# Kernel tuning notes

Hardware: AMD Instinct MI355X
Metric: run time of the kernel (lower is better)

## Reference

```python
import jax, jax.numpy as jnp
import numpy as np

B, N, E, F, H = 4, 10000, 320000, 128, 128


def setup_inputs() -> dict:
    key = jax.random.key(0)
    ks = jax.random.split(key, 12)
    s = 1.0 / np.sqrt(F)
    sh = 1.0 / np.sqrt(H)
    return {
        "batch_feat": jax.random.normal(ks[0], (B, N, F), dtype=jnp.float32),
        "batch_edges": jax.random.randint(ks[1], (B, 2, E), 0, N, dtype=jnp.int32),
        "batch_attr": jax.random.uniform(ks[2], (B, E), dtype=jnp.float32),
        "W1": jax.random.uniform(ks[3], (F, H), jnp.float32, -s, s),
        "b1": jnp.zeros((H,), jnp.float32),
        "W2": jax.random.uniform(ks[4], (H, H), jnp.float32, -sh, sh),
        "b2": jnp.zeros((H,), jnp.float32),
        "W3": jax.random.uniform(ks[5], (H, H), jnp.float32, -sh, sh),
        "b3": jnp.zeros((H,), jnp.float32),
        "Wl": jax.random.uniform(ks[6], (H, 1), jnp.float32, -sh, sh),
        "bl": jnp.zeros((1,), jnp.float32),
    }


def reference(batch_feat, batch_edges, batch_attr, W1, b1, W2, b2, W3, b3, Wl, bl):
    n_nodes = batch_feat.shape[1]

    def gcn_conv(x, row, col, w, W, b):
        # PyG gcn_norm with add_self_loops=False: deg = scatter_add(w, col)
        deg = jax.ops.segment_sum(w, col, num_segments=n_nodes)  # [N]
        dinv = jnp.where(deg > 0, jax.lax.rsqrt(deg), 0.0)
        norm = dinv[row] * w * dinv[col]                         # [E]
        xw = x @ W                                               # [N,H]
        msg = norm[:, None] * xw[row]                            # gather [E,H]
        return jax.ops.segment_sum(msg, col, num_segments=n_nodes) + b

    def per_graph(x, ei, w):
        row, col = ei[0], ei[1]
        h = jax.nn.relu(gcn_conv(x, row, col, w, W1, b1))
        h = jax.nn.relu(gcn_conv(h, row, col, w, W2, b2))
        h = jax.nn.relu(gcn_conv(h, row, col, w, W3, b3))
        return h.mean(axis=0) @ Wl + bl                          # [1]

    return jax.vmap(per_graph)(batch_feat, batch_edges, batch_attr)  # [B,1]
```

## Files before the change

### kernel.cpp

```cpp
#include <hip/hip_runtime.h>

#define BB 4
#define NN 10000
#define EE 320000
#define HH 128
#define HALFN 5000
#define NK2 (2 * NN)
#define RS (2 * NN + 1)
#define NHB 64
#define EPB (EE / NHB)

__global__ __launch_bounds__(256) void hist_kernel(
    const int* __restrict__ edges, unsigned short* __restrict__ hb,
    unsigned short* __restrict__ lrank) {
  __shared__ int lh[NN];
  int b = blockIdx.y;
  int blk = blockIdx.x;
  int t = threadIdx.x;
  const int* rows = edges + (size_t)b * 2 * EE;
  const int* cols = rows + EE;
#pragma unroll
  for (int half = 0; half < 2; ++half) {
    for (int i = t; i < NN; i += 256) lh[i] = 0;
    __syncthreads();
    for (int i = t; i < EPB; i += 256) {
      int e = blk * EPB + i;
      int row = rows[e];
      int col = cols[e];
      if ((row >= HALFN) == (half != 0)) {
        int lr = atomicAdd(&lh[col], 1);
        lrank[(size_t)b * EE + e] = (unsigned short)lr;
      }
    }
    __syncthreads();
    unsigned short* hbrow = hb + ((size_t)(b * NHB + blk)) * NK2 + half * NN;
    for (int i = t; i < NN; i += 256) hbrow[i] = (unsigned short)lh[i];
    __syncthreads();
  }
}

__global__ __launch_bounds__(256) void colscan_kernel(
    unsigned short* __restrict__ hb, int* __restrict__ cnt) {
  int b = blockIdx.y;
  int k = blockIdx.x * 256 + threadIdx.x;
  if (k >= NK2) return;
  int acc = 0;
  for (int j = 0; j < NHB; ++j) {
    size_t idx = ((size_t)(b * NHB + j)) * NK2 + k;
    int v = hb[idx];
    hb[idx] = (unsigned short)acc;
    acc += v;
  }
  cnt[b * NK2 + k] = acc;
}

__global__ __launch_bounds__(256) void scan_kernel(
    const int* __restrict__ cnt, int* __restrict__ rowstart) {
  int b = blockIdx.x, t = threadIdx.x;
  __shared__ int s[256];
  int running = 0;
  for (int base = 0; base < NK2; base += 2048) {
    int v[8];
    int i0 = base + t * 8;
    int tsum = 0;
#pragma unroll
    for (int j = 0; j < 8; ++j) {
      v[j] = (i0 + j < NK2) ? cnt[b * NK2 + i0 + j] : 0;
      tsum += v[j];
    }
    s[t] = tsum;
    __syncthreads();
    for (int o = 1; o < 256; o <<= 1) {
      int add = (t >= o) ? s[t - o] : 0;
      __syncthreads();
      s[t] += add;
      __syncthreads();
    }
    int ex = running + s[t] - tsum;
#pragma unroll
    for (int j = 0; j < 8; ++j) {
      if (i0 + j < NK2) rowstart[b * RS + i0 + j] = ex;
      ex += v[j];
    }
    int tot = s[255];
    __syncthreads();
    running += tot;
  }
  if (t == 0) rowstart[b * RS + NK2] = running;
}

__global__ __launch_bounds__(256) void fill_kernel(
    const int* __restrict__ edges, const float* __restrict__ attr,
    const unsigned short* __restrict__ lrank, const unsigned short* __restrict__ hb,
    const int* __restrict__ rowstart, int2* __restrict__ csr) {
  int b = blockIdx.y;
  int e0 = (blockIdx.x * 256 + threadIdx.x) * 2;
  int blk = e0 / EPB;
  int2 rr = *(const int2*)(edges + (size_t)b * 2 * EE + e0);
  int2 cc = *(const int2*)(edges + (size_t)b * 2 * EE + EE + e0);
  float2 ww = *(const float2*)(attr + (size_t)b * EE + e0);
  unsigned int lr2 = *(const unsigned int*)(lrank + (size_t)b * EE + e0);
  int k0 = ((rr.x >= HALFN) ? NN : 0) + cc.x;
  int k1 = ((rr.y >= HALFN) ? NN : 0) + cc.y;
  const unsigned short* hbrow = hb + ((size_t)(b * NHB + blk)) * NK2;
  int p0 = rowstart[b * RS + k0] + (int)hbrow[k0] + (int)(lr2 & 0xffffu);
  int p1 = rowstart[b * RS + k1] + (int)hbrow[k1] + (int)(lr2 >> 16);
  csr[(size_t)b * EE + p0] = make_int2(rr.x, __float_as_int(ww.x));
  csr[(size_t)b * EE + p1] = make_int2(rr.y, __float_as_int(ww.y));
}

__global__ __launch_bounds__(256) void deg_kernel(
    const int2* __restrict__ csr, const int* __restrict__ rowstart,
    float* __restrict__ dinv) {
  int b = blockIdx.y;
  int n = blockIdx.x * 256 + threadIdx.x;
  if (n >= NN) return;
  const int2* c = csr + (size_t)b * EE;
  float sum = 0.f;
#pragma unroll
  for (int q = 0; q < 2; ++q) {
    int key = q * NN + n;
    int s0 = rowstart[b * RS + key], s1 = rowstart[b * RS + key + 1];
    for (int i = s0; i < s1; ++i) sum += __int_as_float(c[i].y);
  }
  dinv[b * NN + n] = sum > 0.f ? rsqrtf(sum) : 0.f;
}

__global__ __launch_bounds__(256) void gemm_kernel(
    const float* __restrict__ xsrc, const float* __restrict__ p0,
    const float* __restrict__ p1, const float* __restrict__ dinv,
    const float* __restrict__ xbias, const float* __restrict__ W,
    float* __restrict__ out, int fused) {
  __shared__ float xs[32 * 68];
  __shared__ float ws[32 * 144];
  int b = blockIdx.y;
  int row0 = blockIdx.x * 64;
  int t = threadIdx.x;
  int rg = t >> 4, cg = t & 15;
  int fc = cg * 8 + ((cg >> 2) << 2);
  float acc[4][8];
#pragma unroll
  for (int r = 0; r < 4; ++r)
#pragma unroll
    for (int j = 0; j < 8; ++j) acc[r][j] = 0.f;
  size_t gbase = (size_t)b * NN * HH;

  for (int k0 = 0; k0 < HH; k0 += 32) {
#pragma unroll
    for (int i = 0; i < 2; ++i) {
      int idx = t + i * 256;
      int rl = idx >> 3, kq = idx & 7;
      int row = row0 + rl;
      float4 v = make_float4(0.f, 0.f, 0.f, 0.f);
      if (row < NN) {
        size_t o = gbase + (size_t)row * HH + k0 + kq * 4;
        if (fused) {
          float4 u0 = *(const float4*)(p0 + o);
          float4 u1 = *(const float4*)(p1 + o);
          float dn = dinv[b * NN + row];
          float4 bb = *(const float4*)(xbias + k0 + kq * 4);
          v.x = fmaxf((u0.x + u1.x) * dn + bb.x, 0.f);
          v.y = fmaxf((u0.y + u1.y) * dn + bb.y, 0.f);
          v.z = fmaxf((u0.z + u1.z) * dn + bb.z, 0.f);
          v.w = fmaxf((u0.w + u1.w) * dn + bb.w, 0.f);
        } else {
          v = *(const float4*)(xsrc + o);
        }
      }
      xs[(kq * 4 + 0) * 68 + rl] = v.x;
      xs[(kq * 4 + 1) * 68 + rl] = v.y;
      xs[(kq * 4 + 2) * 68 + rl] = v.z;
      xs[(kq * 4 + 3) * 68 + rl] = v.w;
    }
#pragma unroll
    for (int i = 0; i < 4; ++i) {
      int idx = t + i * 256;
      int kk = idx >> 5, c = (idx & 31) * 4;
      float4 v = *(const float4*)(W + (size_t)(k0 + kk) * HH + c);
      int f = c + ((c >> 5) << 2);
      *(float4*)&ws[kk * 144 + f] = v;
    }
    __syncthreads();
#pragma unroll 4
    for (int k = 0; k < 32; ++k) {
      float4 xv = *(const float4*)&xs[k * 68 + rg * 4];
      float4 w0 = *(const float4*)&ws[k * 144 + fc];
      float4 w1 = *(const float4*)&ws[k * 144 + fc + 4];
      const float* xp = (const float*)&xv;
#pragma unroll
      for (int r = 0; r < 4; ++r) {
        acc[r][0] += xp[r] * w0.x; acc[r][1] += xp[r] * w0.y;
        acc[r][2] += xp[r] * w0.z; acc[r][3] += xp[r] * w0.w;
        acc[r][4] += xp[r] * w1.x; acc[r][5] += xp[r] * w1.y;
        acc[r][6] += xp[r] * w1.z; acc[r][7] += xp[r] * w1.w;
      }
    }
    __syncthreads();
  }
#pragma unroll
  for (int r = 0; r < 4; ++r) {
    int row = row0 + rg * 4 + r;
    if (row < NN) {
      float* og = out + gbase + (size_t)row * HH + cg * 8;
      *(float4*)og = make_float4(acc[r][0], acc[r][1], acc[r][2], acc[r][3]);
      *(float4*)(og + 4) = make_float4(acc[r][4], acc[r][5], acc[r][6], acc[r][7]);
    }
  }
}

__global__ __launch_bounds__(256) void agg_kernel(
    const float* __restrict__ xw, const int2* __restrict__ csr,
    const int* __restrict__ rowstart, const float* __restrict__ dinv,
    float* __restrict__ p0g, float* __restrict__ p1g) {
  int g = blockIdx.x & 7;
  int b = g >> 1;
  int q = g & 1;
  int chunk = blockIdx.x >> 3;
  int half = (threadIdx.x >> 5) & 1;
  int n = chunk * 8 + (threadIdx.x >> 6) * 2 + half;
  int sl = threadIdx.x & 31;
  int key = q * NN + n;
  int s0 = rowstart[b * RS + key], s1 = rowstart[b * RS + key + 1];
  const float* xwg = xw + (size_t)b * NN * HH;
  const float* dv = dinv + b * NN;
  const int2* c = csr + (size_t)b * EE;
  float4 a0 = make_float4(0.f, 0.f, 0.f, 0.f);
  float4 a1 = make_float4(0.f, 0.f, 0.f, 0.f);
  float4 a2 = make_float4(0.f, 0.f, 0.f, 0.f);
  float4 a3 = make_float4(0.f, 0.f, 0.f, 0.f);
  int i = s0;
  for (; i + 4 <= s1; i += 4) {
    int2 e0 = c[i];
    int2 e1 = c[i + 1];
    int2 e2 = c[i + 2];
    int2 e3 = c[i + 3];
    float w0 = __int_as_float(e0.y) * dv[e0.x];
    float w1 = __int_as_float(e1.y) * dv[e1.x];
    float w2 = __int_as_float(e2.y) * dv[e2.x];
    float w3 = __int_as_float(e3.y) * dv[e3.x];
    float4 v0 = *(const float4*)(xwg + (size_t)e0.x * HH + sl * 4);
    float4 v1 = *(const float4*)(xwg + (size_t)e1.x * HH + sl * 4);
    float4 v2 = *(const float4*)(xwg + (size_t)e2.x * HH + sl * 4);
    float4 v3 = *(const float4*)(xwg + (size_t)e3.x * HH + sl * 4);
    a0.x += w0 * v0.x; a0.y += w0 * v0.y; a0.z += w0 * v0.z; a0.w += w0 * v0.w;
    a1.x += w1 * v1.x; a1.y += w1 * v1.y; a1.z += w1 * v1.z; a1.w += w1 * v1.w;
    a2.x += w2 * v2.x; a2.y += w2 * v2.y; a2.z += w2 * v2.z; a2.w += w2 * v2.w;
    a3.x += w3 * v3.x; a3.y += w3 * v3.y; a3.z += w3 * v3.z; a3.w += w3 * v3.w;
  }
  for (; i < s1; ++i) {
    int2 e0 = c[i];
    float w0 = __int_as_float(e0.y) * dv[e0.x];
    float4 v0 = *(const float4*)(xwg + (size_t)e0.x * HH + sl * 4);
    a0.x += w0 * v0.x; a0.y += w0 * v0.y; a0.z += w0 * v0.z; a0.w += w0 * v0.w;
  }
  a0.x += a1.x + a2.x + a3.x;
  a0.y += a1.y + a2.y + a3.y;
  a0.z += a1.z + a2.z + a3.z;
  a0.w += a1.w + a2.w + a3.w;
  float* pq = (q == 0) ? p0g : p1g;
  *(float4*)(pq + ((size_t)b * NN + n) * HH + sl * 4) = a0;
}

__global__ __launch_bounds__(64) void init_out_kernel(float* out, const float* __restrict__ bl) {
  if (threadIdx.x < BB) out[threadIdx.x] = bl[0];
}

__global__ __launch_bounds__(256) void final_kernel(
    const float* __restrict__ p0g, const float* __restrict__ p1g,
    const float* __restrict__ dinv, const float* __restrict__ b3,
    const float* __restrict__ Wl, float* __restrict__ out) {
  int b = blockIdx.y;
  int t = threadIdx.x;
  int f = t & 127;
  int rr = t >> 7;
  float bf = b3[f];
  const float* dv = dinv + b * NN;
  float p = 0.f;
  for (int n = blockIdx.x * 2 + rr; n < NN; n += gridDim.x * 2) {
    size_t o = ((size_t)b * NN + n) * HH + f;
    p += fmaxf((p0g[o] + p1g[o]) * dv[n] + bf, 0.f);
  }
  __shared__ float s[256];
  s[t] = p;
  __syncthreads();
  float v = 0.f;
  if (t < 128) v = (s[t] + s[t + 128]) * Wl[f];
  __syncthreads();
  s[t] = v;
  __syncthreads();
  for (int o = 64; o > 0; o >>= 1) {
    if (t < o) s[t] += s[t + o];
    __syncthreads();
  }
  if (t == 0) atomicAdd(&out[b], s[0] * (1.0f / NN));
}

extern "C" void kernel_launch(void* const* d_in, const int* in_sizes, int n_in,
                              void* d_out, int out_size, void* d_ws, size_t ws_size,
                              hipStream_t stream) {
  const float* feat = (const float*)d_in[0];
  const int* edges = (const int*)d_in[1];
  const float* attr = (const float*)d_in[2];
  const float* W1 = (const float*)d_in[3];
  const float* b1 = (const float*)d_in[4];
  const float* W2 = (const float*)d_in[5];
  const float* b2 = (const float*)d_in[6];
  const float* W3 = (const float*)d_in[7];
  const float* b3 = (const float*)d_in[8];
  const float* Wl = (const float*)d_in[9];
  const float* bl = (const float*)d_in[10];
  float* out = (float*)d_out;

  char* ws = (char*)d_ws;
  size_t off = 0;
  auto alloc = [&](size_t bytes) {
    size_t o = off;
    off = (off + bytes + 255) & ~(size_t)255;
    return o;
  };
  int*   cnt      = (int*)  (ws + alloc((size_t)BB * NK2 * 4));
  int*   rowstart = (int*)  (ws + alloc((size_t)BB * RS * 4));
  int2*  csr      = (int2*) (ws + alloc((size_t)BB * EE * 8));
  float* xw       = (float*)(ws + alloc((size_t)BB * NN * HH * 4));
  float* p0       = (float*)(ws + alloc((size_t)BB * NN * HH * 4));
  float* p1       = (float*)(ws + alloc((size_t)BB * NN * HH * 4));
  unsigned short* lrank = (unsigned short*)xw;
  unsigned short* hb    = (unsigned short*)p0;
  float* dinv = (float*)cnt;

  dim3 hgrid(NHB, BB);
  hist_kernel<<<hgrid, 256, 0, stream>>>(edges, hb, lrank);
  colscan_kernel<<<dim3((NK2 + 255) / 256, BB), 256, 0, stream>>>(hb, cnt);
  scan_kernel<<<BB, 256, 0, stream>>>(cnt, rowstart);
  dim3 egrid2(EE / 512, BB);
  fill_kernel<<<egrid2, 256, 0, stream>>>(edges, attr, lrank, hb, rowstart, csr);
  deg_kernel<<<dim3((NN + 255) / 256, BB), 256, 0, stream>>>(csr, rowstart, dinv);

  dim3 ggrid((NN + 63) / 64, BB);
  int agrid = 8 * (NN / 8);

  gemm_kernel<<<ggrid, 256, 0, stream>>>(feat, nullptr, nullptr, nullptr, nullptr, W1, xw, 0);
  agg_kernel<<<agrid, 256, 0, stream>>>(xw, csr, rowstart, dinv, p0, p1);
  gemm_kernel<<<ggrid, 256, 0, stream>>>(nullptr, p0, p1, dinv, b1, W2, xw, 1);
  agg_kernel<<<agrid, 256, 0, stream>>>(xw, csr, rowstart, dinv, p0, p1);
  gemm_kernel<<<ggrid, 256, 0, stream>>>(nullptr, p0, p1, dinv, b2, W3, xw, 1);
  agg_kernel<<<agrid, 256, 0, stream>>>(xw, csr, rowstart, dinv, p0, p1);

  init_out_kernel<<<1, 64, 0, stream>>>(out, bl);
  final_kernel<<<dim3(64, BB), 256, 0, stream>>>(p0, p1, dinv, b3, Wl, out);
}
```

Before: 347.0 us.

## Compute degree during histogram, prefold dinv into CSR weights, use nontemporal access

```diff
diff --git a/kernel.cpp b/kernel.cpp
--- a/kernel.cpp
+++ b/kernel.cpp
@@ -10,52 +10,66 @@
 #define NHB 64
 #define EPB (EE / NHB)
 
+typedef int i32x2 __attribute__((ext_vector_type(2)));
+typedef float f32x4 __attribute__((ext_vector_type(4)));
+
 __global__ __launch_bounds__(256) void hist_kernel(
-    const int* __restrict__ edges, unsigned short* __restrict__ hb,
+    const int* __restrict__ edges, const float* __restrict__ attr,
+    unsigned short* __restrict__ hb, float* __restrict__ wsp,
     unsigned short* __restrict__ lrank) {
   __shared__ int lh[NN];
-  int b = blockIdx.y;
-  int blk = blockIdx.x;
-  int t = threadIdx.x;
+  __shared__ float lw[NN];
+  int b = blockIdx.y, blk = blockIdx.x, t = threadIdx.x;
   const int* rows = edges + (size_t)b * 2 * EE;
   const int* cols = rows + EE;
+  const float* wa = attr + (size_t)b * EE;
 #pragma unroll
   for (int half = 0; half < 2; ++half) {
-    for (int i = t; i < NN; i += 256) lh[i] = 0;
+    for (int i = t; i < NN; i += 256) { lh[i] = 0; lw[i] = 0.f; }
     __syncthreads();
     for (int i = t; i < EPB; i += 256) {
       int e = blk * EPB + i;
       int row = rows[e];
-      int col = cols[e];
       if ((row >= HALFN) == (half != 0)) {
+        int col = cols[e];
         int lr = atomicAdd(&lh[col], 1);
+        atomicAdd(&lw[col], wa[e]);
         lrank[(size_t)b * EE + e] = (unsigned short)lr;
       }
     }
     __syncthreads();
     unsigned short* hbrow = hb + ((size_t)(b * NHB + blk)) * NK2 + half * NN;
-    for (int i = t; i < NN; i += 256) hbrow[i] = (unsigned short)lh[i];
+    float* wsrow = wsp + ((size_t)(b * NHB + blk)) * NK2 + half * NN;
+    for (int i = t; i < NN; i += 256) {
+      hbrow[i] = (unsigned short)lh[i];
+      wsrow[i] = lw[i];
+    }
     __syncthreads();
   }
 }
 
 __global__ __launch_bounds__(256) void colscan_kernel(
-    unsigned short* __restrict__ hb, int* __restrict__ cnt) {
+    unsigned short* __restrict__ hb, const float* __restrict__ wsp,
+    int* __restrict__ cnt, float* __restrict__ wtot) {
   int b = blockIdx.y;
   int k = blockIdx.x * 256 + threadIdx.x;
   if (k >= NK2) return;
   int acc = 0;
+  float f = 0.f;
   for (int j = 0; j < NHB; ++j) {
     size_t idx = ((size_t)(b * NHB + j)) * NK2 + k;
     int v = hb[idx];
     hb[idx] = (unsigned short)acc;
     acc += v;
+    f += wsp[idx];
   }
   cnt[b * NK2 + k] = acc;
+  wtot[b * NK2 + k] = f;
 }
 
 __global__ __launch_bounds__(256) void scan_kernel(
-    const int* __restrict__ cnt, int* __restrict__ rowstart) {
+    const int* __restrict__ cnt, const float* __restrict__ wtot,
+    int* __restrict__ rowstart, float* __restrict__ dinv) {
   int b = blockIdx.x, t = threadIdx.x;
   __shared__ int s[256];
   int running = 0;
@@ -87,12 +101,17 @@
     running += tot;
   }
   if (t == 0) rowstart[b * RS + NK2] = running;
+  for (int i = t; i < NN; i += 256) {
+    float sm = wtot[b * NK2 + i] + wtot[b * NK2 + NN + i];
+    dinv[b * NN + i] = sm > 0.f ? rsqrtf(sm) : 0.f;
+  }
 }
 
 __global__ __launch_bounds__(256) void fill_kernel(
     const int* __restrict__ edges, const float* __restrict__ attr,
     const unsigned short* __restrict__ lrank, const unsigned short* __restrict__ hb,
-    const int* __restrict__ rowstart, int2* __restrict__ csr) {
+    const int* __restrict__ rowstart, const float* __restrict__ dinv,
+    int2* __restrict__ csr) {
   int b = blockIdx.y;
   int e0 = (blockIdx.x * 256 + threadIdx.x) * 2;
   int blk = e0 / EPB;
@@ -105,25 +124,12 @@
   const unsigned short* hbrow = hb + ((size_t)(b * NHB + blk)) * NK2;
   int p0 = rowstart[b * RS + k0] + (int)hbrow[k0] + (int)(lr2 & 0xffffu);
   int p1 = rowstart[b * RS + k1] + (int)hbrow[k1] + (int)(lr2 >> 16);
-  csr[(size_t)b * EE + p0] = make_int2(rr.x, __float_as_int(ww.x));
-  csr[(size_t)b * EE + p1] = make_int2(rr.y, __float_as_int(ww.y));
-}
-
-__global__ __launch_bounds__(256) void deg_kernel(
-    const int2* __restrict__ csr, const int* __restrict__ rowstart,
-    float* __restrict__ dinv) {
-  int b = blockIdx.y;
-  int n = blockIdx.x * 256 + threadIdx.x;
-  if (n >= NN) return;
-  const int2* c = csr + (size_t)b * EE;
-  float sum = 0.f;
-#pragma unroll
-  for (int q = 0; q < 2; ++q) {
-    int key = q * NN + n;
-    int s0 = rowstart[b * RS + key], s1 = rowstart[b * RS + key + 1];
-    for (int i = s0; i < s1; ++i) sum += __int_as_float(c[i].y);
-  }
-  dinv[b * NN + n] = sum > 0.f ? rsqrtf(sum) : 0.f;
+  float w0 = ww.x * dinv[b * NN + rr.x];
+  float w1 = ww.y * dinv[b * NN + rr.y];
+  i32x2 v0; v0.x = rr.x; v0.y = __float_as_int(w0);
+  i32x2 v1; v1.x = rr.y; v1.y = __float_as_int(w1);
+  __builtin_nontemporal_store(v0, (i32x2*)(csr + (size_t)b * EE + p0));
+  __builtin_nontemporal_store(v1, (i32x2*)(csr + (size_t)b * EE + p1));
 }
 
 __global__ __launch_bounds__(256) void gemm_kernel(
@@ -210,7 +216,7 @@
 
 __global__ __launch_bounds__(256) void agg_kernel(
     const float* __restrict__ xw, const int2* __restrict__ csr,
-    const int* __restrict__ rowstart, const float* __restrict__ dinv,
+    const int* __restrict__ rowstart,
     float* __restrict__ p0g, float* __restrict__ p1g) {
   int g = blockIdx.x & 7;
   int b = g >> 1;
@@ -222,7 +228,6 @@
   int key = q * NN + n;
   int s0 = rowstart[b * RS + key], s1 = rowstart[b * RS + key + 1];
   const float* xwg = xw + (size_t)b * NN * HH;
-  const float* dv = dinv + b * NN;
   const int2* c = csr + (size_t)b * EE;
   float4 a0 = make_float4(0.f, 0.f, 0.f, 0.f);
   float4 a1 = make_float4(0.f, 0.f, 0.f, 0.f);
@@ -230,14 +235,14 @@
   float4 a3 = make_float4(0.f, 0.f, 0.f, 0.f);
   int i = s0;
   for (; i + 4 <= s1; i += 4) {
-    int2 e0 = c[i];
-    int2 e1 = c[i + 1];
-    int2 e2 = c[i + 2];
-    int2 e3 = c[i + 3];
-    float w0 = __int_as_float(e0.y) * dv[e0.x];
-    float w1 = __int_as_float(e1.y) * dv[e1.x];
-    float w2 = __int_as_float(e2.y) * dv[e2.x];
-    float w3 = __int_as_float(e3.y) * dv[e3.x];
+    i32x2 e0 = __builtin_nontemporal_load((const i32x2*)(c + i));
+    i32x2 e1 = __builtin_nontemporal_load((const i32x2*)(c + i + 1));
+    i32x2 e2 = __builtin_nontemporal_load((const i32x2*)(c + i + 2));
+    i32x2 e3 = __builtin_nontemporal_load((const i32x2*)(c + i + 3));
+    float w0 = __int_as_float(e0.y);
+    float w1 = __int_as_float(e1.y);
+    float w2 = __int_as_float(e2.y);
+    float w3 = __int_as_float(e3.y);
     float4 v0 = *(const float4*)(xwg + (size_t)e0.x * HH + sl * 4);
     float4 v1 = *(const float4*)(xwg + (size_t)e1.x * HH + sl * 4);
     float4 v2 = *(const float4*)(xwg + (size_t)e2.x * HH + sl * 4);
@@ -248,8 +253,8 @@
     a3.x += w3 * v3.x; a3.y += w3 * v3.y; a3.z += w3 * v3.z; a3.w += w3 * v3.w;
   }
   for (; i < s1; ++i) {
-    int2 e0 = c[i];
-    float w0 = __int_as_float(e0.y) * dv[e0.x];
+    i32x2 e0 = __builtin_nontemporal_load((const i32x2*)(c + i));
+    float w0 = __int_as_float(e0.y);
     float4 v0 = *(const float4*)(xwg + (size_t)e0.x * HH + sl * 4);
     a0.x += w0 * v0.x; a0.y += w0 * v0.y; a0.z += w0 * v0.z; a0.w += w0 * v0.w;
   }
@@ -258,7 +263,8 @@
   a0.z += a1.z + a2.z + a3.z;
   a0.w += a1.w + a2.w + a3.w;
   float* pq = (q == 0) ? p0g : p1g;
-  *(float4*)(pq + ((size_t)b * NN + n) * HH + sl * 4) = a0;
+  __builtin_nontemporal_store(*(const f32x4*)&a0,
+                              (f32x4*)(pq + ((size_t)b * NN + n) * HH + sl * 4));
 }
 
 __global__ __launch_bounds__(64) void init_out_kernel(float* out, const float* __restrict__ bl) {
@@ -320,31 +326,32 @@
   };
   int*   cnt      = (int*)  (ws + alloc((size_t)BB * NK2 * 4));
   int*   rowstart = (int*)  (ws + alloc((size_t)BB * RS * 4));
+  float* wtot     = (float*)(ws + alloc((size_t)BB * NK2 * 4));
+  float* dinv     = (float*)(ws + alloc((size_t)BB * NN * 4));
   int2*  csr      = (int2*) (ws + alloc((size_t)BB * EE * 8));
   float* xw       = (float*)(ws + alloc((size_t)BB * NN * HH * 4));
   float* p0       = (float*)(ws + alloc((size_t)BB * NN * HH * 4));
   float* p1       = (float*)(ws + alloc((size_t)BB * NN * HH * 4));
   unsigned short* lrank = (unsigned short*)xw;
   unsigned short* hb    = (unsigned short*)p0;
-  float* dinv = (float*)cnt;
+  float*          wsp   = (float*)p1;
 
   dim3 hgrid(NHB, BB);
-  hist_kernel<<<hgrid, 256, 0, stream>>>(edges, hb, lrank);
-  colscan_kernel<<<dim3((NK2 + 255) / 256, BB), 256, 0, stream>>>(hb, cnt);
-  scan_kernel<<<BB, 256, 0, stream>>>(cnt, rowstart);
+  hist_kernel<<<hgrid, 256, 0, stream>>>(edges, attr, hb, wsp, lrank);
+  colscan_kernel<<<dim3((NK2 + 255) / 256, BB), 256, 0, stream>>>(hb, wsp, cnt, wtot);
+  scan_kernel<<<BB, 256, 0, stream>>>(cnt, wtot, rowstart, dinv);
   dim3 egrid2(EE / 512, BB);
-  fill_kernel<<<egrid2, 256, 0, stream>>>(edges, attr, lrank, hb, rowstart, csr);
-  deg_kernel<<<dim3((NN + 255) / 256, BB), 256, 0, stream>>>(csr, rowstart, dinv);
+  fill_kernel<<<egrid2, 256, 0, stream>>>(edges, attr, lrank, hb, rowstart, dinv, csr);
 
   dim3 ggrid((NN + 63) / 64, BB);
   int agrid = 8 * (NN / 8);
 
   gemm_kernel<<<ggrid, 256, 0, stream>>>(feat, nullptr, nullptr, nullptr, nullptr, W1, xw, 0);
-  agg_kernel<<<agrid, 256, 0, stream>>>(xw, csr, rowstart, dinv, p0, p1);
+  agg_kernel<<<agrid, 256, 0, stream>>>(xw, csr, rowstart, p0, p1);
   gemm_kernel<<<ggrid, 256, 0, stream>>>(nullptr, p0, p1, dinv, b1, W2, xw, 1);
-  agg_kernel<<<agrid, 256, 0, stream>>>(xw, csr, rowstart, dinv, p0, p1);
+  agg_kernel<<<agrid, 256, 0, stream>>>(xw, csr, rowstart, p0, p1);
   gemm_kernel<<<ggrid, 256, 0, stream>>>(nullptr, p0, p1, dinv, b2, W3, xw, 1);
-  agg_kernel<<<agrid, 256, 0, stream>>>(xw, csr, rowstart, dinv, p0, p1);
+  agg_kernel<<<agrid, 256, 0, stream>>>(xw, csr, rowstart, p0, p1);
 
   init_out_kernel<<<1, 64, 0, stream>>>(out, bl);
   final_kernel<<<dim3(64, BB), 256, 0, stream>>>(p0, p1, dinv, b3, Wl, out);
```

Result: slower. 414.6 us (+19.5%).
